# Kernel tuning notes

Measured on AMD Instinct MI355X. Metric: run time of the kernel, lower is better.

The kernel has to match this reference:

```python
import jax, jax.numpy as jnp
import numpy as np

N_NODES = 50000
N_EDGES = 1600000
IN_DIM = 128
HIDDEN = 16
HEADS = 8
OUT_DIM = 64


def setup_inputs() -> dict:
    key = jax.random.key(0)
    k1, k2, k3, k4, k5 = jax.random.split(key, 5)
    h = jax.random.normal(k1, (N_NODES, IN_DIM), dtype=jnp.float32)
    W1 = jax.random.normal(k2, (IN_DIM, HEADS * HIDDEN), dtype=jnp.float32) * (IN_DIM ** -0.5)
    W2 = jax.random.normal(k3, (HEADS * HIDDEN, OUT_DIM), dtype=jnp.float32) * ((HEADS * HIDDEN) ** -0.5)
    src = jax.random.randint(k4, (N_EDGES,), 0, N_NODES, dtype=jnp.int32)
    dst = jax.random.randint(k5, (N_EDGES,), 0, N_NODES, dtype=jnp.int32)
    return {"h": h, "W1": W1, "W2": W2, "src": src, "dst": dst}


def dot_gat_conv(h, W, src, dst, num_heads, out_feats):
    # Project and split heads: [N, H, D]
    feat = (h @ W).reshape(-1, num_heads, out_feats)
    fs = feat[src]                       # [E, H, D] gather
    fd = feat[dst]                       # [E, H, D] gather
    scale = jnp.asarray(out_feats, feat.dtype) ** -0.5
    e = jnp.einsum('ehd,ehd->eh', fs, fd) * scale  # [E, H] scaled dot score
    # Edge softmax over incoming edges of each destination node
    m = jax.ops.segment_max(e, dst, num_segments=N_NODES)   # [N, H]
    m = jnp.where(jnp.isfinite(m), m, jnp.zeros_like(m))    # isolated nodes
    ex = jnp.exp(e - m[dst])                                 # [E, H]
    denom = jax.ops.segment_sum(ex, dst, num_segments=N_NODES)  # [N, H]
    a = ex / jnp.maximum(denom[dst], jnp.asarray(1e-9, ex.dtype))  # [E, H]
    # Weighted scatter-sum aggregation: [N, H, D]
    return jax.ops.segment_sum(a[:, :, None] * fs, dst, num_segments=N_NODES)


def reference(h, W1, W2, src, dst):
    h1 = dot_gat_conv(h, W1, src, dst, HEADS, HIDDEN)  # [N, H, hidden]
    h1 = jax.nn.elu(h1).reshape(N_NODES, HEADS * HIDDEN)  # flatten(1)
    # Dropout: eval-mode identity
    h2 = dot_gat_conv(h1, W2, src, dst, 1, OUT_DIM)  # [N, 1, out]
    return h2.mean(axis=1)  # [N, out]
```

## Files before the change

kernel.cpp:

```cpp
#include <hip/hip_runtime.h>
#include <hip/hip_bf16.h>

#define N_NODES 50000
#define N_EDGES 1600000
#define EPB 4096
#define NB_A ((N_EDGES + EPB - 1) / EPB)
#define NBUCK2 391
#define BSHIFT 7
#define BMASK 127
#define CAP 8064

typedef short bf16x8 __attribute__((ext_vector_type(8)));
typedef float f32x4  __attribute__((ext_vector_type(4)));
typedef float f32x2  __attribute__((ext_vector_type(2)));

#if __has_builtin(__builtin_amdgcn_exp2f)
#define EXP2(x) __builtin_amdgcn_exp2f(x)
#else
#define EXP2(x) exp2f(x)
#endif
#define LOG2E 1.44269504088896340736f

__device__ __forceinline__ float bf16_raw_to_f32(unsigned short u) {
    return __uint_as_float(((unsigned)u) << 16);
}
__device__ __forceinline__ unsigned short f32_to_bf16_raw(float v) {
    unsigned u = __float_as_uint(v);
    return (unsigned short)((u + 0x7fffu + ((u >> 16) & 1u)) >> 16);
}
__device__ __forceinline__ float load_elem(const void* p, size_t i, int f) {
    if (f) return ((const float*)p)[i];
    return bf16_raw_to_f32(((const unsigned short*)p)[i]);
}
__device__ __forceinline__ void unpack8v(uint4 u, f32x2* f) {
    f[0] = (f32x2){__uint_as_float(u.x << 16), __uint_as_float(u.x & 0xffff0000u)};
    f[1] = (f32x2){__uint_as_float(u.y << 16), __uint_as_float(u.y & 0xffff0000u)};
    f[2] = (f32x2){__uint_as_float(u.z << 16), __uint_as_float(u.z & 0xffff0000u)};
    f[3] = (f32x2){__uint_as_float(u.w << 16), __uint_as_float(u.w & 0xffff0000u)};
}

__device__ __forceinline__ int block_detect(const unsigned short* w1raw) {
    __shared__ float red[256];
    int t = threadIdx.x;
    float mx = 0.f;
    for (int i = t * 2; i < 16384; i += 512) {
        float v = fabsf(bf16_raw_to_f32(w1raw[i]));
        if (!isnan(v)) mx = fmaxf(mx, v);
    }
    red[t] = mx;
    __syncthreads();
    for (int s = 128; s > 0; s >>= 1) {
        if (t < s) red[t] = fmaxf(red[t], red[t + s]);
        __syncthreads();
    }
    return (red[0] > 1e4f) ? 1 : 0;
}

#define WPAD 136

__global__ void k1_prep_kernel(const void* __restrict__ W1,
                               const void* __restrict__ W2,
                               unsigned short* __restrict__ W1T,
                               unsigned short* __restrict__ W2T,
                               int* __restrict__ flag) {
    int bid = blockIdx.x;
    if (bid < 12) {
        const int f = block_detect((const unsigned short*)W1);
        int tid = threadIdx.x;
        if (bid < 8) {
            int n = bid * 16 + (tid & 15);
            int kb = (tid >> 4) * 8;
            for (int j = 0; j < 8; ++j)
                W1T[n * WPAD + kb + j] = f32_to_bf16_raw(load_elem(W1, (size_t)(kb + j) * 128 + n, f));
        } else {
            int n = (bid - 8) * 16 + (tid & 15);
            int kb = (tid >> 4) * 8;
            for (int j = 0; j < 8; ++j)
                W2T[n * WPAD + kb + j] = f32_to_bf16_raw(load_elem(W2, (size_t)(kb + j) * 64 + n, f));
        }
    } else {
        int f = block_detect((const unsigned short*)W1);
        if (threadIdx.x == 0) flag[0] = f;
    }
}

__device__ __forceinline__ void gemm1_body(const void* __restrict__ h,
                                           const unsigned short* __restrict__ W1T,
                                           unsigned short* __restrict__ feat1, int N,
                                           int f, int blk, int row_base) {
    int lane = threadIdx.x & 63;
    int rbase = row_base + blk * 64 + (threadIdx.x >> 6) * 16;
    int arow = rbase + (lane & 15);
    int arowc = min(arow, N - 1);
    int kb0 = (lane >> 4) * 8;

    f32x4 acc[8];
#pragma unroll
    for (int t = 0; t < 8; ++t) acc[t] = (f32x4){0.f, 0.f, 0.f, 0.f};

#pragma unroll
    for (int ks = 0; ks < 4; ++ks) {
        int kb = ks * 32 + kb0;
        bf16x8 afrag;
        if (f == 0) {
            afrag = *(const bf16x8*)((const unsigned short*)h + (size_t)arowc * 128 + kb);
        } else {
            const float* hp = (const float*)h + (size_t)arowc * 128 + kb;
#pragma unroll
            for (int j = 0; j < 8; ++j) afrag[j] = (short)f32_to_bf16_raw(hp[j]);
        }
#pragma unroll
        for (int t = 0; t < 8; ++t) {
            int n = t * 16 + (lane & 15);
            bf16x8 bfrag = *(const bf16x8*)(W1T + n * WPAD + kb);
            acc[t] = __builtin_amdgcn_mfma_f32_16x16x32_bf16(afrag, bfrag, acc[t], 0, 0, 0);
        }
    }
    int orow0 = rbase + (lane >> 4) * 4;
    int col = lane & 15;
#pragma unroll
    for (int t = 0; t < 8; ++t)
#pragma unroll
        for (int r = 0; r < 4; ++r) {
            int row = orow0 + r;
            if (row < N)
                feat1[(size_t)row * 128 + t * 16 + col] = f32_to_bf16_raw(acc[t][r]);
        }
}

#define G1LO 391
#define G1OFF (G1LO * 64)

__global__ void k2_binA_gemm1lo_kernel(const int* __restrict__ src,
                                       const int* __restrict__ dst,
                                       int* __restrict__ bcur,
                                       unsigned* __restrict__ inter, int E,
                                       const void* __restrict__ h,
                                       const unsigned short* __restrict__ W1T,
                                       unsigned short* __restrict__ feat1, int N,
                                       const int* __restrict__ flag) {
    int bid = blockIdx.x;
    if (bid >= NB_A) {
        gemm1_body(h, W1T, feat1, N, *flag, bid - NB_A, 0);
        return;
    }
    __shared__ int hist[NBUCK2], gbase[NBUCK2], cur[NBUCK2];
    int t = threadIdx.x;
    for (int i = t; i < NBUCK2; i += 256) { hist[i] = 0; cur[i] = 0; }
    __syncthreads();
    int e0 = bid * EPB;
    for (int k = 0; k < 16; ++k) {
        int e = e0 + k * 256 + t;
        if (e < E) atomicAdd(&hist[dst[e] >> BSHIFT], 1);
    }
    __syncthreads();
    for (int i = t; i < NBUCK2; i += 256) {
        int hv = hist[i];
        gbase[i] = hv ? (i * CAP + atomicAdd(&bcur[i], hv)) : 0;
    }
    __syncthreads();
    for (int k = 0; k < 16; ++k) {
        int e = e0 + k * 256 + t;
        if (e < E) {
            int d = dst[e];
            int b = d >> BSHIFT;
            int off = atomicAdd(&cur[b], 1);
            int slot = gbase[b] + off;
            if (slot < (b + 1) * CAP)
                inter[slot] = (unsigned)src[e] | ((unsigned)(d & BMASK) << 16);
        }
    }
}

__global__ void k3_binB_gemm1hi_kernel(unsigned* __restrict__ inter,
                                       const int* __restrict__ bcur,
                                       int* __restrict__ start,
                                       int* __restrict__ endv,
                                       int N, int E,
                                       const void* __restrict__ h,
                                       const unsigned short* __restrict__ W1T,
                                       unsigned short* __restrict__ feat1,
                                       const int* __restrict__ flag) {
    int bid = blockIdx.x;
    if (bid >= NBUCK2) {
        gemm1_body(h, W1T, feat1, N, *flag, bid - NBUCK2, G1OFF);
        return;
    }
    int b = bid;
    int node0 = b << BSHIFT;
    __shared__ int ibuf[CAP];
    __shared__ int hist[128];
    __shared__ int tmp[128];
    int t = threadIdx.x;
    int cnt = min(bcur[b], CAP);
    int gb = b * CAP;
    for (int i = t; i < cnt; i += 256) ibuf[i] = (int)inter[gb + i];
    if (t < 128) hist[t] = 0;
    __syncthreads();
    for (int i = t; i < cnt; i += 256) atomicAdd(&hist[((unsigned)ibuf[i]) >> 16], 1);
    __syncthreads();
    int own = (t < 128) ? hist[t] : 0;
    if (t < 128) tmp[t] = own;
    __syncthreads();
    for (int off = 1; off < 128; off <<= 1) {
        int x = (t >= off && t < 128) ? tmp[t - off] : 0;
        __syncthreads();
        if (t < 128) tmp[t] += x;
        __syncthreads();
    }
    int nodeCnt = min(128, N - node0);
    int sbase = gb + ((t < 128) ? (tmp[t] - own) : 0);
    if (t < nodeCnt) { start[node0 + t] = sbase; endv[node0 + t] = sbase + own; }
    if (t < 128) hist[t] = sbase;
    __syncthreads();
    for (int i = t; i < cnt; i += 256) {
        unsigned u = (unsigned)ibuf[i];
        int slot = atomicAdd(&hist[u >> 16], 1);
        inter[slot] = u & 0xffffu;
    }
}

#define GAT1_PROC(U0, U1)                                                     \
    {                                                                         \
        f32x2 f0[4], f1[4];                                                   \
        unpack8v(U0, f0); unpack8v(U1, f1);                                   \
        f32x2 p0 = fd2[0] * f0[0];                                            \
        f32x2 p1 = fd2[0] * f1[0];                                            \
        _Pragma("unroll")                                                     \
        for (int k = 1; k < 4; ++k) { p0 += fd2[k] * f0[k]; p1 += fd2[k] * f1[k]; } \
        float q0 = p0.x + p0.y, q1 = p1.x + p1.y;                             \
        q0 += __shfl_xor(q0, 1); q1 += __shfl_xor(q1, 1);                     \
        float w0 = EXP2(q0), w1 = EXP2(q1);                                   \
        f32x2 W0 = (f32x2){w0, w0}, W1 = (f32x2){w1, w1};                     \
        _Pragma("unroll")                                                     \
        for (int k = 0; k < 4; ++k) { acc2[k] += W0 * f0[k]; acc2[k] += W1 * f1[k]; } \
        l += w0 + w1;                                                         \
    }

__global__ void gat1_kernel(const unsigned short* __restrict__ feat1,
                            const int* __restrict__ csr_src,
                            const int* __restrict__ start,
                            const int* __restrict__ endv,
                            const unsigned short* __restrict__ W2T,
                            unsigned short* __restrict__ feat2, int N) {
    __shared__ float aggl[4][128];
    int widx = threadIdx.x >> 6;
    int wave = blockIdx.x * 4 + widx;
    bool act = wave < N;
    int lane = threadIdx.x & 63;
    int grp = lane >> 4, gl = lane & 15;
    const char* fb = (const char*)feat1;
    unsigned loff = (unsigned)gl << 4;
    unsigned wrow = act ? ((unsigned)wave << 8) : 0u;
    f32x2 fd2[4];
    unpack8v(*(const uint4*)(fb + (wrow + loff)), fd2);
    const float SC = 0.25f * LOG2E;
    const f32x2 SC2 = (f32x2){SC, SC};
#pragma unroll
    for (int k = 0; k < 4; ++k) fd2[k] *= SC2;

    float l = 0.f;
    f32x2 acc2[4];
#pragma unroll
    for (int k = 0; k < 4; ++k) acc2[k] = (f32x2){0.f, 0.f};

    int e0 = act ? start[wave] : 0, e1 = act ? endv[wave] : 0;
    int nfull = (e1 - e0) >> 3;
    int base = e0;
    uint4 a0, a1, b0, b1;
    if (nfull > 0) {
        int s0 = csr_src[base + grp];
        int s1 = csr_src[base + 4 + grp];
        a0 = *(const uint4*)(fb + (((unsigned)s0 << 8) + loff));
        a1 = *(const uint4*)(fb + (((unsigned)s1 << 8) + loff));
    }
    if (nfull > 1) {
        int s0 = csr_src[base + 8 + grp];
        int s1 = csr_src[base + 12 + grp];
        b0 = *(const uint4*)(fb + (((unsigned)s0 << 8) + loff));
        b1 = *(const uint4*)(fb + (((unsigned)s1 << 8) + loff));
    }
    for (int it = 0; it + 2 < nfull; ++it) {
        int nb = base + 16;
        int s0 = csr_src[nb + grp];
        int s1 = csr_src[nb + 4 + grp];
        uint4 n0 = *(const uint4*)(fb + (((unsigned)s0 << 8) + loff));
        uint4 n1 = *(const uint4*)(fb + (((unsigned)s1 << 8) + loff));
        GAT1_PROC(a0, a1);
        a0 = b0; a1 = b1; b0 = n0; b1 = n1;
        base += 8;
    }
    if (nfull > 1) { GAT1_PROC(a0, a1); a0 = b0; a1 = b1; base += 8; }
    if (nfull > 0) { GAT1_PROC(a0, a1); base += 8; }
    for (; base < e1; base += 4) {
        int ed = base + grp;
        bool eact = ed < e1;
        int s = eact ? csr_src[ed] : 0;
        uint4 u = *(const uint4*)(fb + (((unsigned)s << 8) + loff));
        f32x2 fv[4]; unpack8v(u, fv);
        f32x2 p = fd2[0] * fv[0];
#pragma unroll
        for (int k = 1; k < 4; ++k) p += fd2[k] * fv[k];
        float q = p.x + p.y;
        q += __shfl_xor(q, 1);
        float w = eact ? EXP2(q) : 0.f;
        f32x2 W = (f32x2){w, w};
#pragma unroll
        for (int k = 0; k < 4; ++k) acc2[k] += W * fv[k];
        l += w;
    }
#pragma unroll
    for (int off = 16; off <= 32; off <<= 1) {
        l += __shfl_xor(l, off);
#pragma unroll
        for (int k = 0; k < 4; ++k) {
            acc2[k].x += __shfl_xor(acc2[k].x, off);
            acc2[k].y += __shfl_xor(acc2[k].y, off);
        }
    }
    if (grp == 0) {
        float rcp = 1.f / fmaxf(l, 1e-9f);
#pragma unroll
        for (int k = 0; k < 4; ++k) {
            float x0 = acc2[k].x * rcp;
            float x1 = acc2[k].y * rcp;
            x0 = (x0 > 0.f) ? x0 : expm1f(x0);
            x1 = (x1 > 0.f) ? x1 : expm1f(x1);
            aggl[widx][gl * 8 + 2 * k]     = x0;
            aggl[widx][gl * 8 + 2 * k + 1] = x1;
        }
    }
    __syncthreads();
    if (act) {
        const unsigned short* w2row = W2T + lane * WPAD;
        float acc = 0.f;
#pragma unroll
        for (int kb = 0; kb < 128; kb += 8) {
            bf16x8 wv = *(const bf16x8*)(w2row + kb);
            f32x4 aA = *(const f32x4*)&aggl[widx][kb];
            f32x4 aB = *(const f32x4*)&aggl[widx][kb + 4];
            acc += aA[0] * bf16_raw_to_f32((unsigned short)wv[0]);
            acc += aA[1] * bf16_raw_to_f32((unsigned short)wv[1]);
            acc += aA[2] * bf16_raw_to_f32((unsigned short)wv[2]);
            acc += aA[3] * bf16_raw_to_f32((unsigned short)wv[3]);
            acc += aB[0] * bf16_raw_to_f32((unsigned short)wv[4]);
            acc += aB[1] * bf16_raw_to_f32((unsigned short)wv[5]);
            acc += aB[2] * bf16_raw_to_f32((unsigned short)wv[6]);
            acc += aB[3] * bf16_raw_to_f32((unsigned short)wv[7]);
        }
        feat2[(size_t)wave * 64 + lane] = f32_to_bf16_raw(acc);
    }
}

#define GAT2_PROC(U0, U1)                                                     \
    {                                                                         \
        f32x2 f0[4], f1[4];                                                   \
        unpack8v(U0, f0); unpack8v(U1, f1);                                   \
        f32x2 p0 = fd2[0] * f0[0];                                            \
        f32x2 p1 = fd2[0] * f1[0];                                            \
        _Pragma("unroll")                                                     \
        for (int k = 1; k < 4; ++k) { p0 += fd2[k] * f0[k]; p1 += fd2[k] * f1[k]; } \
        float q0 = p0.x + p0.y, q1 = p1.x + p1.y;                             \
        q0 += __shfl_xor(q0, 1); q1 += __shfl_xor(q1, 1);                     \
        q0 += __shfl_xor(q0, 2); q1 += __shfl_xor(q1, 2);                     \
        q0 += __shfl_xor(q0, 4); q1 += __shfl_xor(q1, 4);                     \
        float w0 = EXP2(q0), w1 = EXP2(q1);                                   \
        f32x2 W0 = (f32x2){w0, w0}, W1 = (f32x2){w1, w1};                     \
        _Pragma("unroll")                                                     \
        for (int k = 0; k < 4; ++k) { acc2[k] += W0 * f0[k]; acc2[k] += W1 * f1[k]; } \
        l += w0 + w1;                                                         \
    }

__global__ void gat2_kernel(const unsigned short* __restrict__ feat2,
                            const int* __restrict__ csr_src,
                            const int* __restrict__ start,
                            const int* __restrict__ endv,
                            void* __restrict__ out, int N,
                            const int* __restrict__ flag) {
    int wave = blockIdx.x * 4 + (threadIdx.x >> 6);
    if (wave >= N) return;
    int lane = threadIdx.x & 63;
    int grp = lane >> 3, gl = lane & 7;
    const int f = *flag;
    const char* fb = (const char*)feat2;
    unsigned loff = (unsigned)gl << 4;
    f32x2 fd2[4];
    unpack8v(*(const uint4*)(fb + (((unsigned)wave << 7) + loff)), fd2);
    const float SC = 0.125f * LOG2E;
    const f32x2 SC2 = (f32x2){SC, SC};
#pragma unroll
    for (int k = 0; k < 4; ++k) fd2[k] *= SC2;

    float l = 0.f;
    f32x2 acc2[4];
#pragma unroll
    for (int k = 0; k < 4; ++k) acc2[k] = (f32x2){0.f, 0.f};

    int e0 = start[wave], e1 = endv[wave];
    int nfull = (e1 - e0) >> 4;
    int base = e0;
    uint4 a0, a1, b0, b1;
    if (nfull > 0) {
        int s0 = csr_src[base + grp];
        int s1 = csr_src[base + 8 + grp];
        a0 = *(const uint4*)(fb + (((unsigned)s0 << 7) + loff));
        a1 = *(const uint4*)(fb + (((unsigned)s1 << 7) + loff));
    }
    if (nfull > 1) {
        int s0 = csr_src[base + 16 + grp];
        int s1 = csr_src[base + 24 + grp];
        b0 = *(const uint4*)(fb + (((unsigned)s0 << 7) + loff));
        b1 = *(const uint4*)(fb + (((unsigned)s1 << 7) + loff));
    }
    for (int it = 0; it + 2 < nfull; ++it) {
        int nb = base + 32;
        int s0 = csr_src[nb + grp];
        int s1 = csr_src[nb + 8 + grp];
        uint4 n0 = *(const uint4*)(fb + (((unsigned)s0 << 7) + loff));
        uint4 n1 = *(const uint4*)(fb + (((unsigned)s1 << 7) + loff));
        GAT2_PROC(a0, a1);
        a0 = b0; a1 = b1; b0 = n0; b1 = n1;
        base += 16;
    }
    if (nfull > 1) { GAT2_PROC(a0, a1); a0 = b0; a1 = b1; base += 16; }
    if (nfull > 0) { GAT2_PROC(a0, a1); base += 16; }
    for (; base < e1; base += 8) {
        int ed = base + grp;
        bool act = ed < e1;
        int s = act ? csr_src[ed] : 0;
        uint4 u = *(const uint4*)(fb + (((unsigned)s << 7) + loff));
        f32x2 fv[4]; unpack8v(u, fv);
        f32x2 p = fd2[0] * fv[0];
#pragma unroll
        for (int k = 1; k < 4; ++k) p += fd2[k] * fv[k];
        float q = p.x + p.y;
        q += __shfl_xor(q, 1);
        q += __shfl_xor(q, 2);
        q += __shfl_xor(q, 4);
        float w = act ? EXP2(q) : 0.f;
        f32x2 W = (f32x2){w, w};
#pragma unroll
        for (int k = 0; k < 4; ++k) acc2[k] += W * fv[k];
        l += w;
    }
#pragma unroll
    for (int off = 8; off <= 32; off <<= 1) {
        l += __shfl_xor(l, off);
#pragma unroll
        for (int k = 0; k < 4; ++k) {
            acc2[k].x += __shfl_xor(acc2[k].x, off);
            acc2[k].y += __shfl_xor(acc2[k].y, off);
        }
    }
    if (grp == 0) {
        float rcp = 1.f / fmaxf(l, 1e-9f);
        float v[8];
#pragma unroll
        for (int k = 0; k < 4; ++k) {
            v[2 * k]     = acc2[k].x * rcp;
            v[2 * k + 1] = acc2[k].y * rcp;
        }
        if (f) {
            float* op = (float*)out + (size_t)wave * 64 + gl * 8;
            *(float4*)(op)     = (float4){v[0], v[1], v[2], v[3]};
            *(float4*)(op + 4) = (float4){v[4], v[5], v[6], v[7]};
        } else {
            uint4 pk;
            pk.x = (unsigned)f32_to_bf16_raw(v[0]) | ((unsigned)f32_to_bf16_raw(v[1]) << 16);
            pk.y = (unsigned)f32_to_bf16_raw(v[2]) | ((unsigned)f32_to_bf16_raw(v[3]) << 16);
            pk.z = (unsigned)f32_to_bf16_raw(v[4]) | ((unsigned)f32_to_bf16_raw(v[5]) << 16);
            pk.w = (unsigned)f32_to_bf16_raw(v[6]) | ((unsigned)f32_to_bf16_raw(v[7]) << 16);
            *(uint4*)((unsigned short*)out + (size_t)wave * 64 + gl * 8) = pk;
        }
    }
}

extern "C" void kernel_launch(void* const* d_in, const int* in_sizes, int n_in,
                              void* d_out, int out_size, void* d_ws, size_t ws_size,
                              hipStream_t stream) {
    const void* h  = d_in[0];
    const void* W1 = d_in[1];
    const void* W2 = d_in[2];
    const int* src = (const int*)d_in[3];
    const int* dst = (const int*)d_in[4];

    float* ws = (float*)d_ws;
    unsigned short* feat1 = (unsigned short*)ws;
    unsigned* inter       = (unsigned*)(ws + 3200000);
    int*   csr_src        = (int*)inter;
    unsigned short* feat2 = (unsigned short*)(ws + 6400000);
    int*   start          = (int*)(ws + 8000000);
    int*   endv           = (int*)(ws + 8060000);
    int*   flag           = (int*)(ws + 8120000);
    int*   bcur           = (int*)(ws + 8121000);
    unsigned short* W1T   = (unsigned short*)(ws + 8130000);
    unsigned short* W2T   = (unsigned short*)(ws + 8140000);

    hipMemsetAsync(bcur, 0, NBUCK2 * sizeof(int), stream);

    k1_prep_kernel<<<13, 256, 0, stream>>>(W1, W2, W1T, W2T, flag);

    k2_binA_gemm1lo_kernel<<<NB_A + G1LO, 256, 0, stream>>>(
        src, dst, bcur, inter, N_EDGES, h, W1T, feat1, N_NODES, flag);

    k3_binB_gemm1hi_kernel<<<NBUCK2 + G1LO, 256, 0, stream>>>(
        inter, bcur, start, endv, N_NODES, N_EDGES, h, W1T, feat1, flag);

    gat1_kernel<<<(N_NODES + 3) / 4, 256, 0, stream>>>(
        feat1, csr_src, start, endv, W2T, feat2, N_NODES);

    gat2_kernel<<<(N_NODES + 3) / 4, 256, 0, stream>>>(
        feat2, csr_src, start, endv, d_out, N_NODES, flag);
}
```

Before: 266.6 us.

## Split second-layer projection out of gat1 into separate MFMA GEMM kernel

The per-node 128x64 projection that gat1 did with scalar FMAs over an LDS buffer is removed. gat1 now writes the ELU-activated layer-1 aggregate to a new bf16 workspace buffer, and a new kernel multiplies it by W2 using bf16 MFMA 16x16x32 instructions. This takes the scalar GEMV, the shared memory and the block barrier out of the gather-bound kernel. In exchange it adds one kernel launch and a 12.8 MB round trip through memory, plus an extra bf16 rounding of the intermediate values.

```diff
diff --git a/kernel.cpp b/kernel.cpp
--- a/kernel.cpp
+++ b/kernel.cpp
@@ -220,6 +220,42 @@
     }
 }
 
+__global__ void gemm2_mfma_kernel(const unsigned short* __restrict__ agg1e,
+                                  const unsigned short* __restrict__ W2T,
+                                  unsigned short* __restrict__ feat2, int N) {
+    int lane = threadIdx.x & 63;
+    int rbase = blockIdx.x * 64 + (threadIdx.x >> 6) * 16;
+    int arow = rbase + (lane & 15);
+    int arowc = min(arow, N - 1);
+    int kb0 = (lane >> 4) * 8;
+
+    f32x4 acc[4];
+#pragma unroll
+    for (int t = 0; t < 4; ++t) acc[t] = (f32x4){0.f, 0.f, 0.f, 0.f};
+
+#pragma unroll
+    for (int ks = 0; ks < 4; ++ks) {
+        int kb = ks * 32 + kb0;
+        bf16x8 afrag = *(const bf16x8*)(agg1e + (size_t)arowc * 128 + kb);
+#pragma unroll
+        for (int t = 0; t < 4; ++t) {
+            int n = t * 16 + (lane & 15);
+            bf16x8 bfrag = *(const bf16x8*)(W2T + n * WPAD + kb);
+            acc[t] = __builtin_amdgcn_mfma_f32_16x16x32_bf16(afrag, bfrag, acc[t], 0, 0, 0);
+        }
+    }
+    int orow0 = rbase + (lane >> 4) * 4;
+    int col = lane & 15;
+#pragma unroll
+    for (int t = 0; t < 4; ++t)
+#pragma unroll
+        for (int r = 0; r < 4; ++r) {
+            int row = orow0 + r;
+            if (row < N)
+                feat2[(size_t)row * 64 + t * 16 + col] = f32_to_bf16_raw(acc[t][r]);
+        }
+}
+
 #define GAT1_PROC(U0, U1)                                                     \
     {                                                                         \
         f32x2 f0[4], f1[4];                                                   \
@@ -241,19 +277,15 @@
                             const int* __restrict__ csr_src,
                             const int* __restrict__ start,
                             const int* __restrict__ endv,
-                            const unsigned short* __restrict__ W2T,
-                            unsigned short* __restrict__ feat2, int N) {
-    __shared__ float aggl[4][128];
-    int widx = threadIdx.x >> 6;
-    int wave = blockIdx.x * 4 + widx;
-    bool act = wave < N;
+                            unsigned short* __restrict__ agg1e, int N) {
+    int wave = blockIdx.x * 4 + (threadIdx.x >> 6);
+    if (wave >= N) return;
     int lane = threadIdx.x & 63;
     int grp = lane >> 4, gl = lane & 15;
     const char* fb = (const char*)feat1;
     unsigned loff = (unsigned)gl << 4;
-    unsigned wrow = act ? ((unsigned)wave << 8) : 0u;
     f32x2 fd2[4];
-    unpack8v(*(const uint4*)(fb + (wrow + loff)), fd2);
+    unpack8v(*(const uint4*)(fb + (((unsigned)wave << 8) + loff)), fd2);
     const float SC = 0.25f * LOG2E;
     const f32x2 SC2 = (f32x2){SC, SC};
 #pragma unroll
@@ -264,7 +296,7 @@
 #pragma unroll
     for (int k = 0; k < 4; ++k) acc2[k] = (f32x2){0.f, 0.f};
 
-    int e0 = act ? start[wave] : 0, e1 = act ? endv[wave] : 0;
+    int e0 = start[wave], e1 = endv[wave];
     int nfull = (e1 - e0) >> 3;
     int base = e0;
     uint4 a0, a1, b0, b1;
@@ -294,8 +326,8 @@
     if (nfull > 0) { GAT1_PROC(a0, a1); base += 8; }
     for (; base < e1; base += 4) {
         int ed = base + grp;
-        bool eact = ed < e1;
-        int s = eact ? csr_src[ed] : 0;
+        bool act = ed < e1;
+        int s = act ? csr_src[ed] : 0;
         uint4 u = *(const uint4*)(fb + (((unsigned)s << 8) + loff));
         f32x2 fv[4]; unpack8v(u, fv);
         f32x2 p = fd2[0] * fv[0];
@@ -303,7 +335,7 @@
         for (int k = 1; k < 4; ++k) p += fd2[k] * fv[k];
         float q = p.x + p.y;
         q += __shfl_xor(q, 1);
-        float w = eact ? EXP2(q) : 0.f;
+        float w = act ? EXP2(q) : 0.f;
         f32x2 W = (f32x2){w, w};
 #pragma unroll
         for (int k = 0; k < 4; ++k) acc2[k] += W * fv[k];
@@ -320,35 +352,20 @@
     }
     if (grp == 0) {
         float rcp = 1.f / fmaxf(l, 1e-9f);
+        float v[8];
 #pragma unroll
         for (int k = 0; k < 4; ++k) {
             float x0 = acc2[k].x * rcp;
             float x1 = acc2[k].y * rcp;
-            x0 = (x0 > 0.f) ? x0 : expm1f(x0);
-            x1 = (x1 > 0.f) ? x1 : expm1f(x1);
-            aggl[widx][gl * 8 + 2 * k]     = x0;
-            aggl[widx][gl * 8 + 2 * k + 1] = x1;
-        }
-    }
-    __syncthreads();
-    if (act) {
-        const unsigned short* w2row = W2T + lane * WPAD;
-        float acc = 0.f;
-#pragma unroll
-        for (int kb = 0; kb < 128; kb += 8) {
-            bf16x8 wv = *(const bf16x8*)(w2row + kb);
-            f32x4 aA = *(const f32x4*)&aggl[widx][kb];
-            f32x4 aB = *(const f32x4*)&aggl[widx][kb + 4];
-            acc += aA[0] * bf16_raw_to_f32((unsigned short)wv[0]);
-            acc += aA[1] * bf16_raw_to_f32((unsigned short)wv[1]);
-            acc += aA[2] * bf16_raw_to_f32((unsigned short)wv[2]);
-            acc += aA[3] * bf16_raw_to_f32((unsigned short)wv[3]);
-            acc += aB[0] * bf16_raw_to_f32((unsigned short)wv[4]);
-            acc += aB[1] * bf16_raw_to_f32((unsigned short)wv[5]);
-            acc += aB[2] * bf16_raw_to_f32((unsigned short)wv[6]);
-            acc += aB[3] * bf16_raw_to_f32((unsigned short)wv[7]);
-        }
-        feat2[(size_t)wave * 64 + lane] = f32_to_bf16_raw(acc);
+            v[2 * k]     = (x0 > 0.f) ? x0 : expm1f(x0);
+            v[2 * k + 1] = (x1 > 0.f) ? x1 : expm1f(x1);
+        }
+        uint4 pk;
+        pk.x = (unsigned)f32_to_bf16_raw(v[0]) | ((unsigned)f32_to_bf16_raw(v[1]) << 16);
+        pk.y = (unsigned)f32_to_bf16_raw(v[2]) | ((unsigned)f32_to_bf16_raw(v[3]) << 16);
+        pk.z = (unsigned)f32_to_bf16_raw(v[4]) | ((unsigned)f32_to_bf16_raw(v[5]) << 16);
+        pk.w = (unsigned)f32_to_bf16_raw(v[6]) | ((unsigned)f32_to_bf16_raw(v[7]) << 16);
+        *(uint4*)(agg1e + (size_t)wave * 128 + gl * 8) = pk;
     }
 }
 
@@ -488,13 +505,14 @@
     unsigned short* feat1 = (unsigned short*)ws;
     unsigned* inter       = (unsigned*)(ws + 3200000);
     int*   csr_src        = (int*)inter;
-    unsigned short* feat2 = (unsigned short*)(ws + 6400000);
-    int*   start          = (int*)(ws + 8000000);
-    int*   endv           = (int*)(ws + 8060000);
-    int*   flag           = (int*)(ws + 8120000);
-    int*   bcur           = (int*)(ws + 8121000);
-    unsigned short* W1T   = (unsigned short*)(ws + 8130000);
-    unsigned short* W2T   = (unsigned short*)(ws + 8140000);
+    unsigned short* agg1e = (unsigned short*)(ws + 6400000);
+    unsigned short* feat2 = (unsigned short*)(ws + 9600000);
+    int*   start          = (int*)(ws + 11200000);
+    int*   endv           = (int*)(ws + 11260000);
+    int*   flag           = (int*)(ws + 11330000);
+    int*   bcur           = (int*)(ws + 11331000);
+    unsigned short* W1T   = (unsigned short*)(ws + 11340000);
+    unsigned short* W2T   = (unsigned short*)(ws + 11350000);
 
     hipMemsetAsync(bcur, 0, NBUCK2 * sizeof(int), stream);
 
@@ -507,8 +525,9 @@
         inter, bcur, start, endv, N_NODES, N_EDGES, h, W1T, feat1, flag);
 
     gat1_kernel<<<(N_NODES + 3) / 4, 256, 0, stream>>>(
-        feat1, csr_src, start, endv, W2T, feat2, N_NODES);
-
+        feat1, csr_src, start, endv, agg1e, N_NODES);
+    gemm2_mfma_kernel<<<(N_NODES + 63) / 64, 256, 0, stream>>>(
+        agg1e, W2T, feat2, N_NODES);
     gat2_kernel<<<(N_NODES + 3) / 4, 256, 0, stream>>>(
         feat2, csr_src, start, endv, d_out, N_NODES, flag);
 }
```

Measured after the change: 239.7 us, median of 2. -10.1%, faster.
